# Kernel optimization log

Hardware: AMD Instinct MI355X
Metric: run time of the kernel (lower is better)

## Reference

```python
import jax, jax.numpy as jnp
import numpy as np

EPS = 1e-5
B, S, D = 4, 2048, 128
BALL_SCALE = 0.05  # keeps points inside the unit Poincare ball for c=1


def setup_inputs() -> dict:
    key = jax.random.key(0)
    kq, kk, kv = jax.random.split(key, 3)
    q = jax.random.normal(kq, (B, S, D), dtype=jnp.float32) * BALL_SCALE
    k = jax.random.normal(kk, (B, S, D), dtype=jnp.float32) * BALL_SCALE
    v_tangent = jax.random.normal(kv, (B, S, D), dtype=jnp.float32)
    c = jnp.asarray(1.0, dtype=jnp.float32)
    beta = jnp.asarray(0.0, dtype=jnp.float32)            # nn.Parameter init 0.0
    attention_bias = jnp.asarray(0.0, dtype=jnp.float32)  # nn.Parameter init 0.0
    return {"q": q, "k": k, "v_tangent": v_tangent, "c": c,
            "beta": beta, "attention_bias": attention_bias}


def reference(q, k, v_tangent, c, beta, attention_bias):
    sqrt_c = jnp.sqrt(c)

    # --- pairwise Poincare distance (all fp32, as in the torch autocast block) ---
    x_norm_sq = jnp.sum(q * q, axis=-1, keepdims=True)            # (B,S,1)
    y_norm_sq = jnp.sum(k * k, axis=-1, keepdims=True)            # (B,S,1)
    xy_dot = jnp.einsum('bsd,btd->bst', q, k)                     # (B,S,S)
    y_norm_sq_t = jnp.swapaxes(y_norm_sq, -2, -1)                 # (B,1,S)
    diff_norm_sq = x_norm_sq - 2.0 * xy_dot + y_norm_sq_t         # ||x-y||^2, (B,S,S)
    denom = (1.0 - c * x_norm_sq) * (1.0 - c * y_norm_sq_t)       # (B,S,S)
    arg = 1.0 + 2.0 * c * diff_norm_sq / jnp.maximum(denom, EPS)
    dist = jnp.arccosh(jnp.maximum(arg, 1.0 + EPS)) / sqrt_c      # (B,S,S)

    # --- attention ---
    beta_positive = jax.nn.softplus(beta)
    attention_scores = -beta_positive * dist - attention_bias
    attention_weights = jax.nn.softmax(attention_scores, axis=-1)  # (B,S,S)
    output_tangent = jnp.einsum('bst,btd->bsd', attention_weights, v_tangent)

    # --- exp map at origin ---
    v_norm = jnp.maximum(
        jnp.sqrt(jnp.sum(output_tangent * output_tangent, axis=-1, keepdims=True)), EPS)
    output_hyperbolic = (jnp.tanh(sqrt_c * v_norm) / sqrt_c) * (output_tangent / v_norm)

    return output_hyperbolic, attention_weights
```

## Files before the change

### kernel.cpp

```cpp
#include <hip/hip_runtime.h>
#include <math.h>

#define B_ 4
#define S_ 2048
#define D_ 128
#define EPSF 1e-5f
#define BN 128
#define PSB 272
#define PRS 4128

typedef __attribute__((ext_vector_type(8))) short short8;
typedef __attribute__((ext_vector_type(4))) float f32x4;

static __device__ __forceinline__ unsigned short f2bf(float f) {
    unsigned u = __float_as_uint(f);
    return (unsigned short)((u + 0x7fffu + ((u >> 16) & 1u)) >> 16);
}


__global__ __launch_bounds__(256) void convqk_kernel(const float* __restrict__ q,
                                                     const float* __restrict__ k,
                                                     const float* __restrict__ cp,
                                                     float* __restrict__ qn, float* __restrict__ kn,
                                                     float* __restrict__ lws,
                                                     float2* __restrict__ qng, float2* __restrict__ kng,
                                                     unsigned* __restrict__ Qb, unsigned* __restrict__ Kb) {
    int row = blockIdx.x * 4 + (threadIdx.x >> 6);
    int lane = threadIdx.x & 63;
    const int NR = B_ * S_;
    const float cc = cp[0];
    bool isQ = row < NR;
    int r = isQ ? row : row - NR;
    float2 v = ((const float2*)(isQ ? q : k))[(size_t)r * 64 + lane];
    unsigned pk = (unsigned)f2bf(v.x) | ((unsigned)f2bf(v.y) << 16);
    float nrm = v.x * v.x + v.y * v.y;
#pragma unroll
    for (int m = 1; m <= 32; m <<= 1) nrm += __shfl_xor(nrm, m, 64);
    if (isQ) {
        Qb[(size_t)r * 64 + lane] = pk;
        if (lane == 0) {
            qn[r] = nrm;
            qng[r] = make_float2(nrm, 2.f * cc * __builtin_amdgcn_rcpf(1.f - cc * nrm));
        }
        if (lane == 1) lws[r] = 0.f;
    } else {
        int b = r >> 11, rbk = r & 2047;
        int tile = rbk >> 7, n = rbk & 127;
        Kb[(size_t)b * 131072 + tile * 8192 + (lane >> 4) * 2048 + n * 16 +
           ((lane >> 2) & 3) * 4 + (lane & 3)] = pk;
        if (lane == 0) {
            kn[r] = nrm;
            kng[r] = make_float2(nrm, __builtin_amdgcn_rcpf(1.f - cc * nrm));
        }
    }
}

__global__ __launch_bounds__(256) void convv_kernel(const float* __restrict__ v, uint4* __restrict__ Vtb) {
    __shared__ unsigned short Vs[128 * 132];
    int b = blockIdx.x >> 4;
    int t = blockIdx.x & 15;
    int tid = threadIdx.x;
    const float* src = v + ((size_t)b * S_ + t * 128) * D_;
    int d4 = tid & 31, key0 = tid >> 5;
#pragma unroll
    for (int it = 0; it < 16; ++it) {
        int key = key0 + it * 8;
        float4 f = *(const float4*)(src + (size_t)key * D_ + d4 * 4);
        unsigned short* dst = &Vs[key * 132 + d4 * 4];
        dst[0] = f2bf(f.x); dst[1] = f2bf(f.y); dst[2] = f2bf(f.z); dst[3] = f2bf(f.w);
    }
    __syncthreads();
    uint4* tile = Vtb + (size_t)blockIdx.x * (128 * 16);
    int d = tid & 127;
    int cl = tid >> 7;
#pragma unroll
    for (int it = 0; it < 8; ++it) {
        int c = cl + it * 2;
        int kb = c * 8;
        unsigned short e0 = Vs[(kb + 0) * 132 + d], e1 = Vs[(kb + 1) * 132 + d];
        unsigned short e2 = Vs[(kb + 2) * 132 + d], e3 = Vs[(kb + 3) * 132 + d];
        unsigned short e4 = Vs[(kb + 4) * 132 + d], e5 = Vs[(kb + 5) * 132 + d];
        unsigned short e6 = Vs[(kb + 6) * 132 + d], e7 = Vs[(kb + 7) * 132 + d];
        uint4 o;
        o.x = (unsigned)e0 | ((unsigned)e1 << 16);
        o.y = (unsigned)e2 | ((unsigned)e3 << 16);
        o.z = (unsigned)e4 | ((unsigned)e5 << 16);
        o.w = (unsigned)e6 | ((unsigned)e7 << 16);
        tile[(c >> 2) * 512 + d * 4 + (c & 3)] = o;
    }
}


__global__ __launch_bounds__(512, 4) void hattn8_kernel(
    const unsigned short* __restrict__ Qb, const char* __restrict__ Kb, const char* __restrict__ Vtb,
    const float2* __restrict__ qng, const float2* __restrict__ kng,
    const float* __restrict__ cp, const float* __restrict__ betap, const float* __restrict__ biasp,
    float* __restrict__ hout, float* __restrict__ wout) {

    __shared__ __align__(1024) char smem[66304];
    float* l_row = (float*)(smem + 66176);
    float* nsq_s = (float*)(smem + 66240);

    const int tid = threadIdx.x;
    const int lane = tid & 63, wave = tid >> 6;
    const int wn = wave;
    const int lm = lane & 15, quad = lane >> 4;

    int xcd = blockIdx.x & 7;
    int b = xcd >> 1;
    int rb = (blockIdx.x >> 3) * 2 + (xcd & 1);
    int s0 = rb * 16;
    const size_t bS = (size_t)b * S_;

    const float beta = betap[0], bias = biasp[0];
    const float cc = cp[0];
    const float beta_pos = fmaxf(beta, 0.f) + log1pf(__expf(-fabsf(beta)));
    const float sqrt_c = sqrtf(cc);
    const float bneg = -beta_pos / sqrt_c;
    const float bias2 = -bias * 1.442695040888963f;
    const float onepe = 1.f + EPSF;

    const char* KbBase = Kb + (size_t)b * 524288;
    const char* VtBase = Vtb + (size_t)b * 16 * 32768;

    if (tid < 16) {
        float2 x = qng[bS + s0 + tid];
        *(float2*)(smem + 66048 + tid * 8) = x;
    } else if (tid < 32) {
        l_row[tid - 16] = 0.f;
    } else if (tid < 48) {
        nsq_s[tid - 32] = 0.f;
    }

    const int n0 = wn * 16 + lm;
    const int foff = n0 * 64 + quad * 16;
    short8 kf[4];
    float2 yg;
    {
#pragma unroll
        for (int ks = 0; ks < 4; ++ks)
            kf[ks] = *(const short8*)(KbBase + ks * 8192 + foff);
        yg = kng[bS + n0];
    }

    short8 aq[4];
    {
        const unsigned short* qrow = Qb + (bS + s0 + lm) * D_;
#pragma unroll
        for (int ks = 0; ks < 4; ++ks)
            aq[ks] = *(const short8*)(qrow + ks * 32 + quad * 8);
    }

    __syncthreads();

    float2 xr4[4];
#pragma unroll
    for (int r = 0; r < 4; ++r)
        xr4[r] = *(const float2*)(smem + 66048 + (quad * 4 + r) * 8);

    f32x4 o = {0.f, 0.f, 0.f, 0.f};
    float lacc[4] = {0.f, 0.f, 0.f, 0.f};

    for (int it = 0; it < 16; ++it) {
        short8 kfn[4], vf[4];
        float2 ygn;
        {
            const char* vb = VtBase + (size_t)it * 32768 + foff;
#pragma unroll
            for (int ks = 0; ks < 4; ++ks)
                vf[ks] = *(const short8*)(vb + ks * 8192);
        }
        if (it < 15) {
            const char* kb = KbBase + (size_t)(it + 1) * 32768 + foff;
#pragma unroll
            for (int ks = 0; ks < 4; ++ks)
                kfn[ks] = *(const short8*)(kb + ks * 8192);
            ygn = kng[bS + (size_t)(it + 1) * 128 + n0];
        }
        __builtin_amdgcn_sched_barrier(0);

        f32x4 acc = {0.f, 0.f, 0.f, 0.f};
#pragma unroll
        for (int ks = 0; ks < 4; ++ks)
            acc = __builtin_amdgcn_mfma_f32_16x16x32_bf16(aq[ks], kf[ks], acc, 0, 0, 0);

#pragma unroll
        for (int r = 0; r < 4; ++r) {
            int row = quad * 4 + r;
            float diff = fmaf(-2.f, acc[r], xr4[r].x + yg.x);
            float arg = fmaf(diff * yg.y, xr4[r].y, 1.f);
            arg = fmaxf(arg, onepe);
            float w = arg + sqrtf(fmaf(arg, arg, -1.f));
            float pv = __builtin_amdgcn_exp2f(fmaf(bneg, __builtin_amdgcn_logf(w), bias2));
            *(unsigned short*)(smem + row * PRS + (it * 128 + n0) * 2) = f2bf(pv);
            lacc[r] += pv;
        }
        __syncthreads();

        {
            const char* prow = smem + lm * PRS + it * 256 + quad * 16;
#pragma unroll
            for (int ks = 0; ks < 4; ++ks) {
                short8 ap = *(const short8*)(prow + ks * 64);
                o = __builtin_amdgcn_mfma_f32_16x16x32_bf16(ap, vf[ks], o, 0, 0, 0);
            }
        }

        if (it < 15) {
#pragma unroll
            for (int ks = 0; ks < 4; ++ks) kf[ks] = kfn[ks];
            yg = ygn;
        }
    }

#pragma unroll
    for (int r = 0; r < 4; ++r) {
        float s = lacc[r];
#pragma unroll
        for (int m = 1; m <= 8; m <<= 1) s += __shfl_xor(s, m, 64);
        if (lm == 0) atomicAdd(&l_row[quad * 4 + r], s);
    }
    __syncthreads();

    float linv[4];
#pragma unroll
    for (int r = 0; r < 4; ++r) linv[r] = 1.f / l_row[quad * 4 + r];

#pragma unroll
    for (int r = 0; r < 4; ++r) {
        float x = o[r] * linv[r];
        o[r] = x;
        float np = x * x;
#pragma unroll
        for (int m = 1; m <= 8; m <<= 1) np += __shfl_xor(np, m, 64);
        if (lm == 0) atomicAdd(&nsq_s[quad * 4 + r], np);
    }
    __syncthreads();
#pragma unroll
    for (int r = 0; r < 4; ++r) {
        int row = quad * 4 + r;
        float vn = fmaxf(sqrtf(nsq_s[row]), EPSF);
        float a = sqrt_c * vn;
        float th = 1.f - 2.f / (__expf(2.f * a) + 1.f);
        float sc = th / a;
        hout[(bS + s0 + row) * D_ + n0] = o[r] * sc;
    }

    {
        float4* wdst = (float4*)(wout + (bS + s0) * (size_t)S_);
#pragma unroll
        for (int j = 0; j < 8; ++j) {
            int idx = tid + j * 512;
            int row = idx >> 8;
            int ch = idx & 255;
            float lr = 1.f / l_row[row];
            uint4 u = *(const uint4*)(smem + row * PRS + ch * 16);
            float4 f0, f1;
            f0.x = __uint_as_float(u.x << 16) * lr;
            f0.y = __uint_as_float(u.x & 0xffff0000u) * lr;
            f0.z = __uint_as_float(u.y << 16) * lr;
            f0.w = __uint_as_float(u.y & 0xffff0000u) * lr;
            f1.x = __uint_as_float(u.z << 16) * lr;
            f1.y = __uint_as_float(u.z & 0xffff0000u) * lr;
            f1.z = __uint_as_float(u.w << 16) * lr;
            f1.w = __uint_as_float(u.w & 0xffff0000u) * lr;
            wdst[idx * 2] = f0;
            wdst[idx * 2 + 1] = f1;
        }
    }
}


__global__ __launch_bounds__(512, 2) void hattn_kernel(
    const unsigned short* __restrict__ Qb, const char* __restrict__ Kb, const char* __restrict__ Vtb,
    const float* __restrict__ qn, const float* __restrict__ kn,
    const float* __restrict__ cp, const float* __restrict__ betap, const float* __restrict__ biasp,
    float* __restrict__ lws, float* __restrict__ houtg, float* __restrict__ woutg) {

    __shared__ __align__(1024) char smem[75136];
    char* KsB = smem;
    char* VtB = smem + 32768;
    char* PsB = smem + 65536;
    float* kn_s  = (float*)(smem + 74240);
    float* qn_s  = (float*)(smem + 74752);
    float* l_row = (float*)(smem + 74880);
    float* nsq_s = (float*)(smem + 75008);

    const int tid = threadIdx.x;
    const int lane = tid & 63, wave = tid >> 6;
    const int wm = wave & 1, wn = wave >> 1;
    const int lm = lane & 15, quad = lane >> 4;

    int xcd = blockIdx.x & 7;
    int b = xcd >> 1;
    int rb = (blockIdx.x >> 3) * 2 + (xcd & 1);
    int s0 = rb * 32;
    const size_t bS = (size_t)b * S_;

    const float cc = cp[0], beta = betap[0], bias = biasp[0];
    const float beta_pos = fmaxf(beta, 0.f) + log1pf(__expf(-fabsf(beta)));
    const float sqrt_c = sqrtf(cc);
    const float inv_sqrt_c = 1.f / sqrt_c;

    if (tid < 32) {
        qn_s[tid] = qn[bS + s0 + tid];
        l_row[tid] = 0.f;
        nsq_s[tid] = 0.f;
    }

    short8 aq[4];
    {
        const unsigned short* qrow = Qb + (bS + s0 + wm * 16 + lm) * D_;
#pragma unroll
        for (int ks = 0; ks < 4; ++ks)
            aq[ks] = *(const short8*)(qrow + ks * 32 + quad * 8);
    }

    f32x4 o0 = {0.f, 0.f, 0.f, 0.f}, o1 = {0.f, 0.f, 0.f, 0.f};

    const char* KbBase = Kb + (size_t)b * 524288;
    const char* VtBase = Vtb + (size_t)b * 16 * 32768;

    for (int t = 0; t < S_ / BN; ++t) {
        int t0 = t * BN;
        __syncthreads();
        {
            const uint4* ksrc = (const uint4*)(KbBase + (size_t)t * 32768);
            const uint4* vsrc = (const uint4*)(VtBase + (size_t)t * 32768);
            uint4* kd = (uint4*)KsB;
            uint4* vd = (uint4*)VtB;
#pragma unroll
            for (int i = 0; i < 4; ++i) {
                kd[tid + i * 512] = ksrc[tid + i * 512];
                vd[tid + i * 512] = vsrc[tid + i * 512];
            }
            if (tid < BN) kn_s[tid] = kn[bS + t0 + tid];
        }
        __syncthreads();

        int n0 = wn * 32 + lm;
        f32x4 acc0 = {0.f, 0.f, 0.f, 0.f}, acc1 = {0.f, 0.f, 0.f, 0.f};
#pragma unroll
        for (int ks = 0; ks < 4; ++ks) {
            short8 b0 = *(const short8*)(KsB + ks * 8192 + n0 * 64 + quad * 16);
            short8 b1 = *(const short8*)(KsB + ks * 8192 + (n0 + 16) * 64 + quad * 16);
            acc0 = __builtin_amdgcn_mfma_f32_16x16x32_bf16(aq[ks], b0, acc0, 0, 0, 0);
            acc1 = __builtin_amdgcn_mfma_f32_16x16x32_bf16(aq[ks], b1, acc1, 0, 0, 0);
        }

        float lp[4];
#pragma unroll
        for (int r = 0; r < 4; ++r) {
            int row = wm * 16 + quad * 4 + r;
            float xn = qn_s[row];
            float fx = 1.f - cc * xn;
            float p0, p1;
#pragma unroll
            for (int nt = 0; nt < 2; ++nt) {
                int col = wn * 32 + nt * 16 + lm;
                float dot = (nt == 0) ? acc0[r] : acc1[r];
                float yn = kn_s[col];
                float diff = xn - 2.f * dot + yn;
                float den = fmaxf(fx * (1.f - cc * yn), EPSF);
                float arg = fmaf(2.f * cc * diff, __builtin_amdgcn_rcpf(den), 1.f);
                arg = fmaxf(arg, 1.f + EPSF);
                float dist = __logf(arg + sqrtf(arg * arg - 1.f)) * inv_sqrt_c;
                float p = __expf(fmaf(-beta_pos, dist, -bias));
                woutg[(bS + s0 + row) * S_ + t0 + col] = p;
                *(unsigned short*)(PsB + row * PSB + col * 2) = f2bf(p);
                if (nt == 0) p0 = p; else p1 = p;
            }
            lp[r] = p0 + p1;
        }
#pragma unroll
        for (int r = 0; r < 4; ++r) {
            float s = lp[r];
#pragma unroll
            for (int m = 1; m <= 8; m <<= 1) s += __shfl_xor(s, m, 64);
            if (lm == 0) atomicAdd(&l_row[wm * 16 + quad * 4 + r], s);
        }
        __syncthreads();

#pragma unroll
        for (int ks = 0; ks < 4; ++ks) {
            short8 ap = *(const short8*)(PsB + (wm * 16 + lm) * PSB + (ks * 32 + quad * 8) * 2);
            int d0 = wn * 32 + lm;
            short8 v0 = *(const short8*)(VtB + ks * 8192 + d0 * 64 + quad * 16);
            short8 v1 = *(const short8*)(VtB + ks * 8192 + (d0 + 16) * 64 + quad * 16);
            o0 = __builtin_amdgcn_mfma_f32_16x16x32_bf16(ap, v0, o0, 0, 0, 0);
            o1 = __builtin_amdgcn_mfma_f32_16x16x32_bf16(ap, v1, o1, 0, 0, 0);
        }
    }
    __syncthreads();

    float xs0[4], xs1[4];
#pragma unroll
    for (int r = 0; r < 4; ++r) {
        int row = wm * 16 + quad * 4 + r;
        float linv = __builtin_amdgcn_rcpf(l_row[row]);
        float x0 = o0[r] * linv, x1 = o1[r] * linv;
        xs0[r] = x0; xs1[r] = x1;
        float np = x0 * x0 + x1 * x1;
#pragma unroll
        for (int m = 1; m <= 8; m <<= 1) np += __shfl_xor(np, m, 64);
        if (lm == 0) atomicAdd(&nsq_s[row], np);
    }
    if (tid < 32) lws[bS + s0 + tid] = l_row[tid];
    __syncthreads();
#pragma unroll
    for (int r = 0; r < 4; ++r) {
        int row = wm * 16 + quad * 4 + r;
        float vn = fmaxf(sqrtf(nsq_s[row]), EPSF);
        float a = sqrt_c * vn;
        float th = 1.f - 2.f * __builtin_amdgcn_rcpf(__expf(2.f * a) + 1.f);
        float sc = th / a;
        houtg[(bS + s0 + row) * D_ + wn * 32 + lm] = xs0[r] * sc;
        houtg[(bS + s0 + row) * D_ + wn * 32 + 16 + lm] = xs1[r] * sc;
    }
}

__global__ __launch_bounds__(256) void wnorm_kernel(float* __restrict__ w,
                                                    const float* __restrict__ lws) {
    size_t idx = (size_t)blockIdx.x * 256 + threadIdx.x;
    int row = (int)(idx >> 9);
    float linv = 1.f / lws[row];
    float4* p = (float4*)w + idx;
    float4 v = *p;
    v.x *= linv; v.y *= linv; v.z *= linv; v.w *= linv;
    *p = v;
}


extern "C" void kernel_launch(void* const* d_in, const int* in_sizes, int n_in,
                              void* d_out, int out_size, void* d_ws, size_t ws_size,
                              hipStream_t stream) {
    const float* q    = (const float*)d_in[0];
    const float* k    = (const float*)d_in[1];
    const float* v    = (const float*)d_in[2];
    const float* c    = (const float*)d_in[3];
    const float* beta = (const float*)d_in[4];
    const float* ab   = (const float*)d_in[5];

    float* out  = (float*)d_out;
    float* hout = out;
    float* wout = out + (size_t)B_ * S_ * D_;

    float* qn  = (float*)d_ws;
    float* kn  = qn + B_ * S_;
    float* lws = kn + B_ * S_;
    char*  wsb = (char*)d_ws;
    const size_t QG_OFF = 98304;
    const size_t KG_OFF = QG_OFF + 65536;
    const size_t QB_OFF = KG_OFF + 65536;
    const size_t KB_OFF = QB_OFF + 2097152;
    const size_t VT_OFF = KB_OFF + 2097152;
    const size_t NEED1  = VT_OFF + 2097152;

    float2*  qng = (float2*)(wsb + QG_OFF);
    float2*  kng = (float2*)(wsb + KG_OFF);
    unsigned* Qb = (unsigned*)(wsb + QB_OFF);
    unsigned* Kb = (unsigned*)(wsb + KB_OFF);
    uint4*   Vtb = (uint4*)(wsb + VT_OFF);

    if (ws_size >= NEED1) {
        convqk_kernel<<<4096, 256, 0, stream>>>(q, k, c, qn, kn, lws, qng, kng, Qb, Kb);
        convv_kernel<<<64, 256, 0, stream>>>(v, Vtb);
        hattn8_kernel<<<512, 512, 0, stream>>>((const unsigned short*)Qb, (const char*)Kb,
                                               (const char*)Vtb, qng, kng, c, beta, ab,
                                               hout, wout);
    } else {
        convqk_kernel<<<4096, 256, 0, stream>>>(q, k, c, qn, kn, lws, qng, kng, Qb, Kb);
        convv_kernel<<<64, 256, 0, stream>>>(v, Vtb);
        hattn_kernel<<<256, 512, 0, stream>>>((const unsigned short*)Qb, (const char*)Kb,
                                              (const char*)Vtb, qn, kn, c, beta, ab,
                                              lws, hout, wout);
        wnorm_kernel<<<(B_ * S_ * S_ / 4) / 256, 256, 0, stream>>>(wout, lws);
    }
}
```

Baseline: 137.8 us.

## Split attention keys across four blocks with partial outputs and bf16 probability staging

Replaces the single-pass attention kernel with a split-K variant. Each block handles 32 query rows and a quarter of the keys, stages K tiles into LDS asynchronously with global_load_lds double buffering, and writes partial outputs plus bf16 unnormalized probabilities to workspace. Separate epilogue kernels then reduce the partials with the exp map and expand the bf16 probabilities into normalized fp32 weights. This is meant to raise occupancy and parallelism, at the cost of extra workspace traffic, global atomics for row sums, and two more launches. The K layout is changed to 64-row tiles to suit the new kernel.

Measured after the change: 181.7 us. 1.32x slower.

```diff
diff --git a/kernel.cpp b/kernel.cpp
--- a/kernel.cpp
+++ b/kernel.cpp
@@ -6,8 +6,8 @@
 #define D_ 128
 #define EPSF 1e-5f
 #define BN 128
-#define PSB 272
 #define PRS 4128
+#define PS2 136
 
 typedef __attribute__((ext_vector_type(8))) short short8;
 typedef __attribute__((ext_vector_type(4))) float f32x4;
@@ -17,14 +17,18 @@
     return (unsigned short)((u + 0x7fffu + ((u >> 16) & 1u)) >> 16);
 }
 
+static __device__ __forceinline__ void gload_lds16(const void* g, void* l) {
+    __builtin_amdgcn_global_load_lds((const __attribute__((address_space(1))) unsigned*)g,
+                                     (__attribute__((address_space(3))) unsigned*)l, 16, 0, 0);
+}
+
 
 __global__ __launch_bounds__(256) void convqk_kernel(const float* __restrict__ q,
                                                      const float* __restrict__ k,
                                                      const float* __restrict__ cp,
-                                                     float* __restrict__ qn, float* __restrict__ kn,
                                                      float* __restrict__ lws,
                                                      float2* __restrict__ qng, float2* __restrict__ kng,
-                                                     unsigned* __restrict__ Qb, unsigned* __restrict__ Kb) {
+                                                     unsigned* __restrict__ Qb, unsigned* __restrict__ KbA) {
     int row = blockIdx.x * 4 + (threadIdx.x >> 6);
     int lane = threadIdx.x & 63;
     const int NR = B_ * S_;
@@ -38,20 +42,16 @@
     for (int m = 1; m <= 32; m <<= 1) nrm += __shfl_xor(nrm, m, 64);
     if (isQ) {
         Qb[(size_t)r * 64 + lane] = pk;
-        if (lane == 0) {
-            qn[r] = nrm;
+        if (lane == 0)
             qng[r] = make_float2(nrm, 2.f * cc * __builtin_amdgcn_rcpf(1.f - cc * nrm));
-        }
         if (lane == 1) lws[r] = 0.f;
     } else {
-        int b = r >> 11, rbk = r & 2047;
-        int tile = rbk >> 7, n = rbk & 127;
-        Kb[(size_t)b * 131072 + tile * 8192 + (lane >> 4) * 2048 + n * 16 +
-           ((lane >> 2) & 3) * 4 + (lane & 3)] = pk;
-        if (lane == 0) {
-            kn[r] = nrm;
+        int b = r >> 11, rloc = r & 2047;
+        int t64 = rloc >> 6, n = rloc & 63;
+        KbA[(size_t)b * 131072 + t64 * 4096 + (lane >> 4) * 1024 + n * 16 +
+            ((lane >> 2) & 3) * 4 + (lane & 3)] = pk;
+        if (lane == 0)
             kng[r] = make_float2(nrm, __builtin_amdgcn_rcpf(1.f - cc * nrm));
-        }
     }
 }
 
@@ -91,25 +91,27 @@
 }
 
 
-__global__ __launch_bounds__(512, 4) void hattn8_kernel(
-    const unsigned short* __restrict__ Qb, const char* __restrict__ Kb, const char* __restrict__ Vtb,
+__global__ __launch_bounds__(512, 6) void hattn11_kernel(
+    const unsigned short* __restrict__ Qb, const char* __restrict__ KbA,
+    const char* __restrict__ Vtb,
     const float2* __restrict__ qng, const float2* __restrict__ kng,
     const float* __restrict__ cp, const float* __restrict__ betap, const float* __restrict__ biasp,
-    float* __restrict__ hout, float* __restrict__ wout) {
-
-    __shared__ __align__(1024) char smem[66304];
-    float* l_row = (float*)(smem + 66176);
-    float* nsq_s = (float*)(smem + 66240);
+    float* __restrict__ lws, float* __restrict__ Opart, uint4* __restrict__ Pws) {
+
+    __shared__ __align__(1024) char smem[37376];
+    char* PsB = smem + 32768;
+    float2* xr_s = (float2*)(smem + 37120);
 
     const int tid = threadIdx.x;
     const int lane = tid & 63, wave = tid >> 6;
-    const int wn = wave;
+    const int wm = wave & 1, wn = wave >> 1;
     const int lm = lane & 15, quad = lane >> 4;
 
-    int xcd = blockIdx.x & 7;
-    int b = xcd >> 1;
-    int rb = (blockIdx.x >> 3) * 2 + (xcd & 1);
-    int s0 = rb * 16;
+    const int qtr = blockIdx.x & 3;
+    const int rid = blockIdx.x >> 2;
+    const int b = rid & 3;
+    const int rb = rid >> 2;
+    const int s0 = rb * 32;
     const size_t bS = (size_t)b * S_;
 
     const float beta = betap[0], bias = biasp[0];
@@ -119,9 +121,197 @@
     const float bneg = -beta_pos / sqrt_c;
     const float bias2 = -bias * 1.442695040888963f;
     const float onepe = 1.f + EPSF;
-
-    const char* KbBase = Kb + (size_t)b * 524288;
-    const char* VtBase = Vtb + (size_t)b * 16 * 32768;
+    (void)sqrt_c;
+
+    const char* KA = KbA + (size_t)b * 524288 + (size_t)qtr * (8 * 16384);
+    const char* Vt = Vtb + (size_t)b * 524288;
+
+    if (tid < 32) xr_s[tid] = qng[bS + s0 + tid];
+
+#pragma unroll
+    for (int j = 0; j < 2; ++j) {
+        int off = (tid + j * 512) * 16;
+        gload_lds16(KA + off, smem + off);
+    }
+
+    short8 aq[4];
+    {
+        const unsigned short* qrow = Qb + (bS + s0 + wm * 16 + lm) * D_;
+#pragma unroll
+        for (int ks = 0; ks < 4; ++ks)
+            aq[ks] = *(const short8*)(qrow + ks * 32 + quad * 8);
+    }
+    __syncthreads();
+
+    f32x4 o0 = {0.f, 0.f, 0.f, 0.f}, o1 = {0.f, 0.f, 0.f, 0.f};
+    float lacc[4] = {0.f, 0.f, 0.f, 0.f};
+    int p = 0;
+    const int col = wn * 16 + lm;
+
+    for (int it = 0; it < 8; ++it) {
+        char* KsC = smem + p * 16384;
+
+        if (it < 7) {
+            const char* ks = KA + (size_t)(it + 1) * 16384;
+            char* kd = smem + (p ^ 1) * 16384;
+#pragma unroll
+            for (int j = 0; j < 2; ++j) {
+                int off = (tid + j * 512) * 16;
+                gload_lds16(ks + off, kd + off);
+            }
+        }
+
+        f32x4 acc = {0.f, 0.f, 0.f, 0.f};
+        {
+            const char* kb = KsC + col * 64 + quad * 16;
+#pragma unroll
+            for (int ks = 0; ks < 4; ++ks) {
+                short8 bk = *(const short8*)(kb + ks * 4096);
+                acc = __builtin_amdgcn_mfma_f32_16x16x32_bf16(aq[ks], bk, acc, 0, 0, 0);
+            }
+        }
+
+        const char* vbase = Vt + (size_t)(qtr * 4 + (it >> 1)) * 32768
+                            + wn * 2048 + lm * 64 + quad * 16;
+        const int kqb = (it & 1) * 2;
+        short8 vf00 = *(const short8*)(vbase + (kqb + 0) * 8192);
+        short8 vf01 = *(const short8*)(vbase + (kqb + 1) * 8192);
+        short8 vf10 = *(const short8*)(vbase + (kqb + 0) * 8192 + 1024);
+        short8 vf11 = *(const short8*)(vbase + (kqb + 1) * 8192 + 1024);
+
+        {
+            float2 yg = kng[bS + qtr * 512 + it * 64 + col];
+#pragma unroll
+            for (int r = 0; r < 4; ++r) {
+                int row = wm * 16 + quad * 4 + r;
+                float2 xr = xr_s[row];
+                float diff = fmaf(-2.f, acc[r], xr.x + yg.x);
+                float arg = fmaxf(fmaf(diff * yg.y, xr.y, 1.f), onepe);
+                float w = arg + sqrtf(fmaf(arg, arg, -1.f));
+                float pv = __builtin_amdgcn_exp2f(fmaf(bneg, __builtin_amdgcn_logf(w), bias2));
+                *(unsigned short*)(PsB + row * PS2 + col * 2) = f2bf(pv);
+                lacc[r] += pv;
+            }
+        }
+        __syncthreads();
+
+        if (tid < 256) {
+            int row = tid >> 3, ch = tid & 7;
+            uint4 u = *(const uint4*)(PsB + row * PS2 + ch * 16);
+            Pws[(((bS + s0 + row) * S_ + qtr * 512 + it * 64) >> 3) + ch] = u;
+        }
+
+        {
+            const char* pr = PsB + (wm * 16 + lm) * PS2 + quad * 16;
+#pragma unroll
+            for (int kq = 0; kq < 2; ++kq) {
+                short8 ap = *(const short8*)(pr + kq * 64);
+                o0 = __builtin_amdgcn_mfma_f32_16x16x32_bf16(ap, kq ? vf01 : vf00, o0, 0, 0, 0);
+                o1 = __builtin_amdgcn_mfma_f32_16x16x32_bf16(ap, kq ? vf11 : vf10, o1, 0, 0, 0);
+            }
+        }
+        __syncthreads();
+        p ^= 1;
+    }
+
+#pragma unroll
+    for (int r = 0; r < 4; ++r) {
+        float s = lacc[r];
+#pragma unroll
+        for (int m = 1; m <= 8; m <<= 1) s += __shfl_xor(s, m, 64);
+        if (lm == 0) atomicAdd(&lws[bS + s0 + wm * 16 + quad * 4 + r], s);
+    }
+
+    float* op = Opart + (size_t)qtr * (B_ * S_ * D_) + (bS + s0) * D_;
+#pragma unroll
+    for (int r = 0; r < 4; ++r) {
+        int row = wm * 16 + quad * 4 + r;
+        op[(size_t)row * D_ + wn * 32 + lm] = o0[r];
+        op[(size_t)row * D_ + wn * 32 + 16 + lm] = o1[r];
+    }
+}
+
+__global__ __launch_bounds__(256) void hepi4_kernel(const float* __restrict__ Opart,
+                                                    const float* __restrict__ lws,
+                                                    const float* __restrict__ cp,
+                                                    float* __restrict__ hout) {
+    int row = blockIdx.x * 4 + (threadIdx.x >> 6);
+    int lane = threadIdx.x & 63;
+    const int NP = B_ * S_ * D_;
+    const float cc = cp[0];
+    const float sqrt_c = sqrtf(cc);
+    float2 a0 = ((const float2*)(Opart + (size_t)row * D_))[lane];
+    float2 a1 = ((const float2*)(Opart + (size_t)NP + (size_t)row * D_))[lane];
+    float2 a2 = ((const float2*)(Opart + (size_t)2 * NP + (size_t)row * D_))[lane];
+    float2 a3 = ((const float2*)(Opart + (size_t)3 * NP + (size_t)row * D_))[lane];
+    float linv = 1.f / lws[row];
+    float x0 = (a0.x + a1.x + a2.x + a3.x) * linv;
+    float x1 = (a0.y + a1.y + a2.y + a3.y) * linv;
+    float np = x0 * x0 + x1 * x1;
+#pragma unroll
+    for (int m = 1; m <= 32; m <<= 1) np += __shfl_xor(np, m, 64);
+    float vn = fmaxf(sqrtf(np), EPSF);
+    float aa = sqrt_c * vn;
+    float t = 1.f - 2.f / (__expf(2.f * aa) + 1.f);
+    float sc = t / aa;
+    float2 o = {x0 * sc, x1 * sc};
+    ((float2*)(hout + (size_t)row * D_))[lane] = o;
+}
+
+__global__ __launch_bounds__(256) void wnorm2_kernel(const uint4* __restrict__ Pws,
+                                                     const float* __restrict__ lws,
+                                                     float* __restrict__ w) {
+    size_t idx = (size_t)blockIdx.x * 256 + threadIdx.x;
+    int row = (int)(idx >> 8);
+    float linv = 1.f / lws[row];
+    uint4 u = Pws[idx];
+    float4 f0, f1;
+    f0.x = __uint_as_float(u.x << 16) * linv;
+    f0.y = __uint_as_float(u.x & 0xffff0000u) * linv;
+    f0.z = __uint_as_float(u.y << 16) * linv;
+    f0.w = __uint_as_float(u.y & 0xffff0000u) * linv;
+    f1.x = __uint_as_float(u.z << 16) * linv;
+    f1.y = __uint_as_float(u.z & 0xffff0000u) * linv;
+    f1.z = __uint_as_float(u.w << 16) * linv;
+    f1.w = __uint_as_float(u.w & 0xffff0000u) * linv;
+    float4* out = (float4*)w + idx * 2;
+    out[0] = f0;
+    out[1] = f1;
+}
+
+
+__global__ __launch_bounds__(512, 4) void hattn8_kernel(
+    const unsigned short* __restrict__ Qb, const char* __restrict__ KbA,
+    const char* __restrict__ Vtb,
+    const float2* __restrict__ qng, const float2* __restrict__ kng,
+    const float* __restrict__ cp, const float* __restrict__ betap, const float* __restrict__ biasp,
+    float* __restrict__ hout, float* __restrict__ wout) {
+
+    __shared__ __align__(1024) char smem[66304];
+    float* l_row = (float*)(smem + 66176);
+    float* nsq_s = (float*)(smem + 66240);
+
+    const int tid = threadIdx.x;
+    const int lane = tid & 63, wave = tid >> 6;
+    const int wn = wave;
+    const int lm = lane & 15, quad = lane >> 4;
+
+    int xcd = blockIdx.x & 7;
+    int b = xcd >> 1;
+    int rb = (blockIdx.x >> 3) * 2 + (xcd & 1);
+    int s0 = rb * 16;
+    const size_t bS = (size_t)b * S_;
+
+    const float beta = betap[0], bias = biasp[0];
+    const float cc = cp[0];
+    const float beta_pos = fmaxf(beta, 0.f) + log1pf(__expf(-fabsf(beta)));
+    const float sqrt_c = sqrtf(cc);
+    const float bneg = -beta_pos / sqrt_c;
+    const float bias2 = -bias * 1.442695040888963f;
+    const float onepe = 1.f + EPSF;
+
+    const char* KA = KbA + (size_t)b * 524288;
+    const char* VtBase = Vtb + (size_t)b * 524288;
 
     if (tid < 16) {
         float2 x = qng[bS + s0 + tid];
@@ -133,13 +323,14 @@
     }
 
     const int n0 = wn * 16 + lm;
-    const int foff = n0 * 64 + quad * 16;
+    const char* kaBase = KA + (n0 >> 6) * 16384 + (n0 & 63) * 64 + quad * 16;
+    const int foffV = n0 * 64 + quad * 16;
     short8 kf[4];
     float2 yg;
     {
 #pragma unroll
         for (int ks = 0; ks < 4; ++ks)
-            kf[ks] = *(const short8*)(KbBase + ks * 8192 + foff);
+            kf[ks] = *(const short8*)(kaBase + ks * 4096);
         yg = kng[bS + n0];
     }
 
@@ -165,16 +356,16 @@
         short8 kfn[4], vf[4];
         float2 ygn;
         {
-            const char* vb = VtBase + (size_t)it * 32768 + foff;
+            const char* vb = VtBase + (size_t)it * 32768 + foffV;
 #pragma unroll
             for (int ks = 0; ks < 4; ++ks)
                 vf[ks] = *(const short8*)(vb + ks * 8192);
         }
         if (it < 15) {
-            const char* kb = KbBase + (size_t)(it + 1) * 32768 + foff;
+            const char* kb = kaBase + (size_t)(it + 1) * 32768;
 #pragma unroll
             for (int ks = 0; ks < 4; ++ks)
-                kfn[ks] = *(const short8*)(kb + ks * 8192);
+                kfn[ks] = *(const short8*)(kb + ks * 4096);
             ygn = kng[bS + (size_t)(it + 1) * 128 + n0];
         }
         __builtin_amdgcn_sched_barrier(0);
@@ -188,8 +379,7 @@
         for (int r = 0; r < 4; ++r) {
             int row = quad * 4 + r;
             float diff = fmaf(-2.f, acc[r], xr4[r].x + yg.x);
-            float arg = fmaf(diff * yg.y, xr4[r].y, 1.f);
-            arg = fmaxf(arg, onepe);
+            float arg = fmaxf(fmaf(diff * yg.y, xr4[r].y, 1.f), onepe);
             float w = arg + sqrtf(fmaf(arg, arg, -1.f));
             float pv = __builtin_amdgcn_exp2f(fmaf(bneg, __builtin_amdgcn_logf(w), bias2));
             *(unsigned short*)(smem + row * PRS + (it * 128 + n0) * 2) = f2bf(pv);
@@ -271,166 +461,6 @@
 }
 
 
-__global__ __launch_bounds__(512, 2) void hattn_kernel(
-    const unsigned short* __restrict__ Qb, const char* __restrict__ Kb, const char* __restrict__ Vtb,
-    const float* __restrict__ qn, const float* __restrict__ kn,
-    const float* __restrict__ cp, const float* __restrict__ betap, const float* __restrict__ biasp,
-    float* __restrict__ lws, float* __restrict__ houtg, float* __restrict__ woutg) {
-
-    __shared__ __align__(1024) char smem[75136];
-    char* KsB = smem;
-    char* VtB = smem + 32768;
-    char* PsB = smem + 65536;
-    float* kn_s  = (float*)(smem + 74240);
-    float* qn_s  = (float*)(smem + 74752);
-    float* l_row = (float*)(smem + 74880);
-    float* nsq_s = (float*)(smem + 75008);
-
-    const int tid = threadIdx.x;
-    const int lane = tid & 63, wave = tid >> 6;
-    const int wm = wave & 1, wn = wave >> 1;
-    const int lm = lane & 15, quad = lane >> 4;
-
-    int xcd = blockIdx.x & 7;
-    int b = xcd >> 1;
-    int rb = (blockIdx.x >> 3) * 2 + (xcd & 1);
-    int s0 = rb * 32;
-    const size_t bS = (size_t)b * S_;
-
-    const float cc = cp[0], beta = betap[0], bias = biasp[0];
-    const float beta_pos = fmaxf(beta, 0.f) + log1pf(__expf(-fabsf(beta)));
-    const float sqrt_c = sqrtf(cc);
-    const float inv_sqrt_c = 1.f / sqrt_c;
-
-    if (tid < 32) {
-        qn_s[tid] = qn[bS + s0 + tid];
-        l_row[tid] = 0.f;
-        nsq_s[tid] = 0.f;
-    }
-
-    short8 aq[4];
-    {
-        const unsigned short* qrow = Qb + (bS + s0 + wm * 16 + lm) * D_;
-#pragma unroll
-        for (int ks = 0; ks < 4; ++ks)
-            aq[ks] = *(const short8*)(qrow + ks * 32 + quad * 8);
-    }
-
-    f32x4 o0 = {0.f, 0.f, 0.f, 0.f}, o1 = {0.f, 0.f, 0.f, 0.f};
-
-    const char* KbBase = Kb + (size_t)b * 524288;
-    const char* VtBase = Vtb + (size_t)b * 16 * 32768;
-
-    for (int t = 0; t < S_ / BN; ++t) {
-        int t0 = t * BN;
-        __syncthreads();
-        {
-            const uint4* ksrc = (const uint4*)(KbBase + (size_t)t * 32768);
-            const uint4* vsrc = (const uint4*)(VtBase + (size_t)t * 32768);
-            uint4* kd = (uint4*)KsB;
-            uint4* vd = (uint4*)VtB;
-#pragma unroll
-            for (int i = 0; i < 4; ++i) {
-                kd[tid + i * 512] = ksrc[tid + i * 512];
-                vd[tid + i * 512] = vsrc[tid + i * 512];
-            }
-            if (tid < BN) kn_s[tid] = kn[bS + t0 + tid];
-        }
-        __syncthreads();
-
-        int n0 = wn * 32 + lm;
-        f32x4 acc0 = {0.f, 0.f, 0.f, 0.f}, acc1 = {0.f, 0.f, 0.f, 0.f};
-#pragma unroll
-        for (int ks = 0; ks < 4; ++ks) {
-            short8 b0 = *(const short8*)(KsB + ks * 8192 + n0 * 64 + quad * 16);
-            short8 b1 = *(const short8*)(KsB + ks * 8192 + (n0 + 16) * 64 + quad * 16);
-            acc0 = __builtin_amdgcn_mfma_f32_16x16x32_bf16(aq[ks], b0, acc0, 0, 0, 0);
-            acc1 = __builtin_amdgcn_mfma_f32_16x16x32_bf16(aq[ks], b1, acc1, 0, 0, 0);
-        }
-
-        float lp[4];
-#pragma unroll
-        for (int r = 0; r < 4; ++r) {
-            int row = wm * 16 + quad * 4 + r;
-            float xn = qn_s[row];
-            float fx = 1.f - cc * xn;
-            float p0, p1;
-#pragma unroll
-            for (int nt = 0; nt < 2; ++nt) {
-                int col = wn * 32 + nt * 16 + lm;
-                float dot = (nt == 0) ? acc0[r] : acc1[r];
-                float yn = kn_s[col];
-                float diff = xn - 2.f * dot + yn;
-                float den = fmaxf(fx * (1.f - cc * yn), EPSF);
-                float arg = fmaf(2.f * cc * diff, __builtin_amdgcn_rcpf(den), 1.f);
-                arg = fmaxf(arg, 1.f + EPSF);
-                float dist = __logf(arg + sqrtf(arg * arg - 1.f)) * inv_sqrt_c;
-                float p = __expf(fmaf(-beta_pos, dist, -bias));
-                woutg[(bS + s0 + row) * S_ + t0 + col] = p;
-                *(unsigned short*)(PsB + row * PSB + col * 2) = f2bf(p);
-                if (nt == 0) p0 = p; else p1 = p;
-            }
-            lp[r] = p0 + p1;
-        }
-#pragma unroll
-        for (int r = 0; r < 4; ++r) {
-            float s = lp[r];
-#pragma unroll
-            for (int m = 1; m <= 8; m <<= 1) s += __shfl_xor(s, m, 64);
-            if (lm == 0) atomicAdd(&l_row[wm * 16 + quad * 4 + r], s);
-        }
-        __syncthreads();
-
-#pragma unroll
-        for (int ks = 0; ks < 4; ++ks) {
-            short8 ap = *(const short8*)(PsB + (wm * 16 + lm) * PSB + (ks * 32 + quad * 8) * 2);
-            int d0 = wn * 32 + lm;
-            short8 v0 = *(const short8*)(VtB + ks * 8192 + d0 * 64 + quad * 16);
-            short8 v1 = *(const short8*)(VtB + ks * 8192 + (d0 + 16) * 64 + quad * 16);
-            o0 = __builtin_amdgcn_mfma_f32_16x16x32_bf16(ap, v0, o0, 0, 0, 0);
-            o1 = __builtin_amdgcn_mfma_f32_16x16x32_bf16(ap, v1, o1, 0, 0, 0);
-        }
-    }
-    __syncthreads();
-
-    float xs0[4], xs1[4];
-#pragma unroll
-    for (int r = 0; r < 4; ++r) {
-        int row = wm * 16 + quad * 4 + r;
-        float linv = __builtin_amdgcn_rcpf(l_row[row]);
-        float x0 = o0[r] * linv, x1 = o1[r] * linv;
-        xs0[r] = x0; xs1[r] = x1;
-        float np = x0 * x0 + x1 * x1;
-#pragma unroll
-        for (int m = 1; m <= 8; m <<= 1) np += __shfl_xor(np, m, 64);
-        if (lm == 0) atomicAdd(&nsq_s[row], np);
-    }
-    if (tid < 32) lws[bS + s0 + tid] = l_row[tid];
-    __syncthreads();
-#pragma unroll
-    for (int r = 0; r < 4; ++r) {
-        int row = wm * 16 + quad * 4 + r;
-        float vn = fmaxf(sqrtf(nsq_s[row]), EPSF);
-        float a = sqrt_c * vn;
-        float th = 1.f - 2.f * __builtin_amdgcn_rcpf(__expf(2.f * a) + 1.f);
-        float sc = th / a;
-        houtg[(bS + s0 + row) * D_ + wn * 32 + lm] = xs0[r] * sc;
-        houtg[(bS + s0 + row) * D_ + wn * 32 + 16 + lm] = xs1[r] * sc;
-    }
-}
-
-__global__ __launch_bounds__(256) void wnorm_kernel(float* __restrict__ w,
-                                                    const float* __restrict__ lws) {
-    size_t idx = (size_t)blockIdx.x * 256 + threadIdx.x;
-    int row = (int)(idx >> 9);
-    float linv = 1.f / lws[row];
-    float4* p = (float4*)w + idx;
-    float4 v = *p;
-    v.x *= linv; v.y *= linv; v.z *= linv; v.w *= linv;
-    *p = v;
-}
-
-
 extern "C" void kernel_launch(void* const* d_in, const int* in_sizes, int n_in,
                               void* d_out, int out_size, void* d_ws, size_t ws_size,
                               hipStream_t stream) {
@@ -445,35 +475,38 @@
     float* hout = out;
     float* wout = out + (size_t)B_ * S_ * D_;
 
-    float* qn  = (float*)d_ws;
-    float* kn  = qn + B_ * S_;
-    float* lws = kn + B_ * S_;
-    char*  wsb = (char*)d_ws;
+    char* wsb = (char*)d_ws;
+    float* lws = (float*)(wsb + 65536);
     const size_t QG_OFF = 98304;
     const size_t KG_OFF = QG_OFF + 65536;
     const size_t QB_OFF = KG_OFF + 65536;
-    const size_t KB_OFF = QB_OFF + 2097152;
-    const size_t VT_OFF = KB_OFF + 2097152;
-    const size_t NEED1  = VT_OFF + 2097152;
+    const size_t KA_OFF = QB_OFF + 2097152;
+    const size_t VT_OFF = KA_OFF + 2097152;
+    const size_t T2_END = VT_OFF + 2097152;
+    const size_t OP_OFF = T2_END;
+    const size_t PW_OFF = OP_OFF + (size_t)4 * B_ * S_ * D_ * 4;
+    const size_t NEED1  = PW_OFF + (size_t)B_ * S_ * S_ * 2;
 
     float2*  qng = (float2*)(wsb + QG_OFF);
     float2*  kng = (float2*)(wsb + KG_OFF);
     unsigned* Qb = (unsigned*)(wsb + QB_OFF);
-    unsigned* Kb = (unsigned*)(wsb + KB_OFF);
+    unsigned* KbA = (unsigned*)(wsb + KA_OFF);
     uint4*   Vtb = (uint4*)(wsb + VT_OFF);
 
+    convqk_kernel<<<4096, 256, 0, stream>>>(q, k, c, lws, qng, kng, Qb, KbA);
+    convv_kernel<<<64, 256, 0, stream>>>(v, Vtb);
+
     if (ws_size >= NEED1) {
-        convqk_kernel<<<4096, 256, 0, stream>>>(q, k, c, qn, kn, lws, qng, kng, Qb, Kb);
-        convv_kernel<<<64, 256, 0, stream>>>(v, Vtb);
-        hattn8_kernel<<<512, 512, 0, stream>>>((const unsigned short*)Qb, (const char*)Kb,
+        float* Opart = (float*)(wsb + OP_OFF);
+        uint4* Pws   = (uint4*)(wsb + PW_OFF);
+        hattn11_kernel<<<1024, 512, 0, stream>>>((const unsigned short*)Qb, (const char*)KbA,
+                                                 (const char*)Vtb, qng, kng, c, beta, ab,
+                                                 lws, Opart, Pws);
+        hepi4_kernel<<<2048, 256, 0, stream>>>(Opart, lws, c, hout);
+        wnorm2_kernel<<<8192, 256, 0, stream>>>(Pws, lws, wout);
+    } else {
+        hattn8_kernel<<<512, 512, 0, stream>>>((const unsigned short*)Qb, (const char*)KbA,
                                                (const char*)Vtb, qng, kng, c, beta, ab,
                                                hout, wout);
-    } else {
-        convqk_kernel<<<4096, 256, 0, stream>>>(q, k, c, qn, kn, lws, qng, kng, Qb, Kb);
-        convv_kernel<<<64, 256, 0, stream>>>(v, Vtb);
-        hattn_kernel<<<256, 512, 0, stream>>>((const unsigned short*)Qb, (const char*)Kb,
-                                              (const char*)Vtb, qn, kn, c, beta, ab,
-                                              lws, hout, wout);
-        wnorm_kernel<<<(B_ * S_ * S_ / 4) / 256, 256, 0, stream>>>(wout, lws);
-    }
-}
+    }
+}
```
